# Performance work log

Hardware: AMD Instinct MI355X
Metric: run time of the kernel (lower is better)

The kernel has to match this reference:

```python
import jax, jax.numpy as jnp
import numpy as np

TEMPERATURE = 0.1
NORMALIZE = True


def setup_inputs() -> dict:
    key = jax.random.key(0)
    k1, k2 = jax.random.split(key)
    B, D = 4096, 512
    return {
        "z_i": jax.random.normal(k1, (B, D), dtype=jnp.float32),
        "z_j": jax.random.normal(k2, (B, D), dtype=jnp.float32),
    }


def _l2norm(x):
    return x / jnp.sqrt(jnp.sum(x * x, axis=-1, keepdims=True))


def reference(z_i, z_j):
    if NORMALIZE:
        z_i = _l2norm(z_i)
        z_j = _l2norm(z_j)
    B = z_i.shape[0]

    inv_t = 1.0 / TEMPERATURE
    logits_aa = (z_i @ z_i.T) * inv_t  # [B, B]
    logits_bb = (z_j @ z_j.T) * inv_t
    logits_ab = (z_i @ z_j.T) * inv_t
    logits_ba = (z_j @ z_i.T) * inv_t

    # Static off-diagonal column indices: row i keeps cols 0..B-1 except i,
    # in ascending order (matches torch boolean-mask row-major extraction).
    j = jnp.arange(B - 1)[None, :]
    i = jnp.arange(B)[:, None]
    idx = j + (j >= i)  # [B, B-1] int32

    take = lambda m: jnp.take_along_axis(m, idx, axis=1)  # [B, B-1]

    pos = jnp.concatenate([jnp.diagonal(logits_ab), jnp.diagonal(logits_ba)])[:, None]  # [2B, 1]
    neg_a = jnp.concatenate([take(logits_aa), take(logits_ab)], axis=1)  # [B, 2(B-1)]
    neg_b = jnp.concatenate([take(logits_ba), take(logits_bb)], axis=1)
    neg = jnp.concatenate([neg_a, neg_b], axis=0)  # [2B, 2(B-1)]

    logits = jnp.concatenate([pos, neg], axis=1)  # [2B, 2B-1]
    logp = jax.nn.log_softmax(logits, axis=1)
    # Original forward uses labels = torch.ones(2B).long() -> target class 1.
    loss = -jnp.mean(logp[:, 1])
    return loss
```

## Files before the change

### kernel.cpp

```cpp
#include <hip/hip_runtime.h>
#include <hip/hip_bf16.h>
#include <hip/hip_fp8.h>


#define BB 4096
#define DD 512
#define NN 8192
#define TILE 128
#define KB 128
#define NBLK 2080

typedef __attribute__((ext_vector_type(4))) float f32x4;

#define AS1 __attribute__((address_space(1)))
#define AS3 __attribute__((address_space(3)))
static __device__ __forceinline__ void gload_lds16(const void* g, void* l) {
    __builtin_amdgcn_global_load_lds((const AS1 void*)g, (AS3 void*)l, 16, 0, 0);
}

__global__ __launch_bounds__(256)
void normalize_kernel(const float* __restrict__ zi, const float* __restrict__ zj,
                      unsigned char* __restrict__ M, float* __restrict__ rowsum) {
    const int wave = threadIdx.x >> 6;
    const int lane = threadIdx.x & 63;
    const int row  = blockIdx.x * 4 + wave;
    if (threadIdx.x < 4) rowsum[blockIdx.x * 4 + threadIdx.x] = 0.f;
    const float* src = (row < BB) ? (zi + (size_t)row * DD)
                                  : (zj + (size_t)(row - BB) * DD);
    float4 v0 = ((const float4*)src)[lane * 2 + 0];
    float4 v1 = ((const float4*)src)[lane * 2 + 1];
    float ss = v0.x*v0.x + v0.y*v0.y + v0.z*v0.z + v0.w*v0.w
             + v1.x*v1.x + v1.y*v1.y + v1.z*v1.z + v1.w*v1.w;
    #pragma unroll
    for (int off = 1; off <= 32; off <<= 1) ss += __shfl_xor(ss, off);
    const float inv = rsqrtf(ss);
    const float vals[8] = {v0.x*inv, v0.y*inv, v0.z*inv, v0.w*inv,
                           v1.x*inv, v1.y*inv, v1.z*inv, v1.w*inv};
    union { long u; unsigned char b[8]; } pk;
    #pragma unroll
    for (int j = 0; j < 8; ++j)
        pk.b[j] = __hip_cvt_float_to_fp8(vals[j], __HIP_SATFINITE, __HIP_E4M3);
    ((long*)(M + (size_t)row * DD))[lane] = pk.u;
}

__global__ __launch_bounds__(256, 4)
void gram_lse_kernel(const unsigned char* __restrict__ Mg,
                     float* __restrict__ rowsum, float* __restrict__ targets) {
    __shared__ __align__(16) char As[TILE * KB];
    __shared__ __align__(16) char Bs[TILE * KB];

    const int d = blockIdx.x;
    const int p = (d & 7) * 260 + (d >> 3);
    int by = (int)((sqrtf(8.0f * (float)p + 1.0f) - 1.0f) * 0.5f);
    while ((by + 1) * (by + 2) / 2 <= p) ++by;
    while (by * (by + 1) / 2 > p) --by;
    const int bx = p - by * (by + 1) / 2;

    const int rowBase = bx * TILE;
    const int colBase = by * TILE;
    const bool diag = (bx == by);
    const int tid  = threadIdx.x;
    const int wave = tid >> 6;
    const int lane = tid & 63;
    const int wr = (wave >> 1) * 64;
    const int wc = (wave & 1) * 64;
    const int l15 = lane & 15;
    const int l4  = lane >> 4;

    const int sg  = (tid & 7) ^ ((tid >> 3) & 7);
    const int sr0 = tid >> 3;
    const unsigned char* gA0 = Mg + (size_t)(rowBase + sr0) * DD + sg * 16;
    const unsigned char* gB0 = Mg + (size_t)(colBase + sr0) * DD + sg * 16;
    char* lA0 = As + tid * 16;
    char* lB0 = Bs + tid * 16;

    const int r7 = l15 & 7;
    const int qh = l4 >> 1, ql = l4 & 1;
    const int aoff0 = (wr + l15) * KB + ql * 8;
    const int boff0 = (wc + l15) * KB + ql * 8;
    const char* BsP = diag ? As : Bs;

    f32x4 acc[4][4] = {};

    for (int k0 = 0; k0 < DD; k0 += KB) {
        __syncthreads();
        #pragma unroll
        for (int i = 0; i < 4; ++i)
            gload_lds16(gA0 + k0 + (size_t)i * 32 * DD, lA0 + i * 4096);
        if (!diag) {
            #pragma unroll
            for (int i = 0; i < 4; ++i)
                gload_lds16(gB0 + k0 + (size_t)i * 32 * DD, lB0 + i * 4096);
        }
        __syncthreads();
        #pragma unroll
        for (int ks = 0; ks < 4; ++ks) {
            const int so = ((((ks << 1) | qh) ^ r7) << 4);
            long a[4], b[4];
            #pragma unroll
            for (int mi = 0; mi < 4; ++mi)
                a[mi] = *(const long*)(As + aoff0 + mi * 2048 + so);
            #pragma unroll
            for (int ni = 0; ni < 4; ++ni)
                b[ni] = *(const long*)(BsP + boff0 + ni * 2048 + so);
            #pragma unroll
            for (int mi = 0; mi < 4; ++mi)
                #pragma unroll
                for (int ni = 0; ni < 4; ++ni)
                    acc[mi][ni] = __builtin_amdgcn_mfma_f32_16x16x32_fp8_fp8(
                        a[mi], b[ni], acc[mi][ni], 0, 0, 0);
        }
    }

    float cs[4] = {0.f, 0.f, 0.f, 0.f};
    #pragma unroll
    for (int mi = 0; mi < 4; ++mi) {
        float rs[4] = {0.f, 0.f, 0.f, 0.f};
        #pragma unroll
        for (int ni = 0; ni < 4; ++ni) {
            const int gcol = colBase + wc + ni * 16 + l15;
            #pragma unroll
            for (int r = 0; r < 4; ++r) {
                const int grow = rowBase + wr + mi * 16 + l4 * 4 + r;
                float logit = 10.f * acc[mi][ni][r];
                float e = __expf(logit - 10.f);
                if (grow == gcol) e = 0.f;
                rs[r] += e;
                cs[ni] += e;
                if (rowBase == 0 && grow < 2) {
                    const int j0 = ((gcol & (BB - 1)) == 0) ? 1 : 0;
                    if (grow == j0) targets[gcol] = logit;
                }
            }
        }
        #pragma unroll
        for (int m = 1; m <= 8; m <<= 1)
            #pragma unroll
            for (int r = 0; r < 4; ++r)
                rs[r] += __shfl_xor(rs[r], m);
        if (l15 == 0) {
            #pragma unroll
            for (int r = 0; r < 4; ++r)
                atomicAdd(&rowsum[rowBase + wr + mi * 16 + l4 * 4 + r], rs[r]);
        }
    }
    if (!diag) {
        #pragma unroll
        for (int ni = 0; ni < 4; ++ni) {
            cs[ni] += __shfl_xor(cs[ni], 16);
            cs[ni] += __shfl_xor(cs[ni], 32);
        }
        if (l4 == 0) {
            #pragma unroll
            for (int ni = 0; ni < 4; ++ni)
                atomicAdd(&rowsum[colBase + wc + ni * 16 + l15], cs[ni]);
        }
    }
}

__global__ __launch_bounds__(1024)
void finalize_kernel(const float* __restrict__ rowsum,
                     const float* __restrict__ targets, float* __restrict__ out) {
    const int tid = threadIdx.x;
    float s = 0.f;
    #pragma unroll
    for (int t = tid; t < NN; t += 1024)
        s += targets[t] - 10.f - __logf(rowsum[t]);
    #pragma unroll
    for (int off = 1; off <= 32; off <<= 1) s += __shfl_xor(s, off);
    __shared__ float red[16];
    if ((tid & 63) == 0) red[tid >> 6] = s;
    __syncthreads();
    if (tid == 0) {
        float t = 0.f;
        #pragma unroll
        for (int i = 0; i < 16; ++i) t += red[i];
        out[0] = -t / (float)NN;
    }
}

extern "C" void kernel_launch(void* const* d_in, const int* in_sizes, int n_in,
                              void* d_out, int out_size, void* d_ws, size_t ws_size,
                              hipStream_t stream) {
    const float* zi = (const float*)d_in[0];
    const float* zj = (const float*)d_in[1];

    unsigned char* M = (unsigned char*)d_ws;
    float* rowsum  = (float*)((char*)d_ws + (size_t)NN * DD);
    float* targets = rowsum + NN;
    float* out = (float*)d_out;

    normalize_kernel<<<NN / 4, 256, 0, stream>>>(zi, zj, M, rowsum);
    gram_lse_kernel<<<NBLK, 256, 0, stream>>>(M, rowsum, targets);
    finalize_kernel<<<1, 1024, 0, stream>>>(rowsum, targets, out);
}
```

Before: 101.0 us.

## Double-buffer LDS tiles in gram kernel and use exp2 in epilogue

Splits the shared-memory A/B tiles into two buffers and prefetches the next K slice with direct global-to-LDS loads while MFMAs consume the current one, removing one barrier per iteration. The epilogue exponential is folded into a single fma plus hardware exp2. Doubling LDS lowers the occupancy bound from 4 to 2 blocks per CU. Correctness relies on the barrier waiting for the async LDS loads to complete.

```diff
diff --git a/kernel.cpp b/kernel.cpp
--- a/kernel.cpp
+++ b/kernel.cpp
@@ -43,11 +43,11 @@
     ((long*)(M + (size_t)row * DD))[lane] = pk.u;
 }
 
-__global__ __launch_bounds__(256, 4)
+__global__ __launch_bounds__(256, 2)
 void gram_lse_kernel(const unsigned char* __restrict__ Mg,
                      float* __restrict__ rowsum, float* __restrict__ targets) {
-    __shared__ __align__(16) char As[TILE * KB];
-    __shared__ __align__(16) char Bs[TILE * KB];
+    __shared__ __align__(16) char As[2][TILE * KB];
+    __shared__ __align__(16) char Bs[2][TILE * KB];
 
     const int d = blockIdx.x;
     const int p = (d & 7) * 260 + (d >> 3);
@@ -71,38 +71,55 @@
     const int sr0 = tid >> 3;
     const unsigned char* gA0 = Mg + (size_t)(rowBase + sr0) * DD + sg * 16;
     const unsigned char* gB0 = Mg + (size_t)(colBase + sr0) * DD + sg * 16;
-    char* lA0 = As + tid * 16;
-    char* lB0 = Bs + tid * 16;
 
     const int r7 = l15 & 7;
     const int qh = l4 >> 1, ql = l4 & 1;
     const int aoff0 = (wr + l15) * KB + ql * 8;
     const int boff0 = (wc + l15) * KB + ql * 8;
-    const char* BsP = diag ? As : Bs;
 
     f32x4 acc[4][4] = {};
 
-    for (int k0 = 0; k0 < DD; k0 += KB) {
+    {
+        char* lA = As[0] + tid * 16;
+        #pragma unroll
+        for (int i = 0; i < 4; ++i)
+            gload_lds16(gA0 + (size_t)i * 32 * DD, lA + i * 4096);
+        if (!diag) {
+            char* lB = Bs[0] + tid * 16;
+            #pragma unroll
+            for (int i = 0; i < 4; ++i)
+                gload_lds16(gB0 + (size_t)i * 32 * DD, lB + i * 4096);
+        }
+    }
+
+    #pragma unroll
+    for (int t = 0; t < DD / KB; ++t) {
         __syncthreads();
-        #pragma unroll
-        for (int i = 0; i < 4; ++i)
-            gload_lds16(gA0 + k0 + (size_t)i * 32 * DD, lA0 + i * 4096);
-        if (!diag) {
+        if (t < DD / KB - 1) {
+            const int k0 = (t + 1) * KB;
+            char* lA = As[(t + 1) & 1] + tid * 16;
             #pragma unroll
             for (int i = 0; i < 4; ++i)
-                gload_lds16(gB0 + k0 + (size_t)i * 32 * DD, lB0 + i * 4096);
-        }
-        __syncthreads();
+                gload_lds16(gA0 + k0 + (size_t)i * 32 * DD, lA + i * 4096);
+            if (!diag) {
+                char* lB = Bs[(t + 1) & 1] + tid * 16;
+                #pragma unroll
+                for (int i = 0; i < 4; ++i)
+                    gload_lds16(gB0 + k0 + (size_t)i * 32 * DD, lB + i * 4096);
+            }
+        }
+        const char* Asrc = As[t & 1];
+        const char* Bsrc = diag ? Asrc : Bs[t & 1];
         #pragma unroll
         for (int ks = 0; ks < 4; ++ks) {
             const int so = ((((ks << 1) | qh) ^ r7) << 4);
             long a[4], b[4];
             #pragma unroll
             for (int mi = 0; mi < 4; ++mi)
-                a[mi] = *(const long*)(As + aoff0 + mi * 2048 + so);
+                a[mi] = *(const long*)(Asrc + aoff0 + mi * 2048 + so);
             #pragma unroll
             for (int ni = 0; ni < 4; ++ni)
-                b[ni] = *(const long*)(BsP + boff0 + ni * 2048 + so);
+                b[ni] = *(const long*)(Bsrc + boff0 + ni * 2048 + so);
             #pragma unroll
             for (int mi = 0; mi < 4; ++mi)
                 #pragma unroll
@@ -112,6 +129,7 @@
         }
     }
 
+    const float C10 = 14.42695040888963f;
     float cs[4] = {0.f, 0.f, 0.f, 0.f};
     #pragma unroll
     for (int mi = 0; mi < 4; ++mi) {
@@ -122,14 +140,13 @@
             #pragma unroll
             for (int r = 0; r < 4; ++r) {
                 const int grow = rowBase + wr + mi * 16 + l4 * 4 + r;
-                float logit = 10.f * acc[mi][ni][r];
-                float e = __expf(logit - 10.f);
+                float e = __builtin_amdgcn_exp2f(fmaf(acc[mi][ni][r], C10, -C10));
                 if (grow == gcol) e = 0.f;
                 rs[r] += e;
                 cs[ni] += e;
                 if (rowBase == 0 && grow < 2) {
                     const int j0 = ((gcol & (BB - 1)) == 0) ? 1 : 0;
-                    if (grow == j0) targets[gcol] = logit;
+                    if (grow == j0) targets[gcol] = 10.f * acc[mi][ni][r];
                 }
             }
         }
```

New measurement: 110.0 us. 8.9% more time.

## Switch Gram kernel to 32x32x64 scaled FP8 MFMA with A in registers

Applied to the files above, without the earlier changes.

Replaces the 16x16x32 FP8 MFMA tiled loop over K with the MI355 32x32x64 f8f6f4 scaled MFMA. The whole 128xD B tile is staged once into LDS with an XOR swizzle, and each wave keeps its 32 A rows in registers loaded straight from global memory, which removes the K-loop barriers and the A LDS traffic. The epilogue uses exp2 with a folded constant. The cost is more registers (occupancy bound dropped to 2) and a larger 64KB LDS footprint.

```diff
diff --git a/kernel.cpp b/kernel.cpp
--- a/kernel.cpp
+++ b/kernel.cpp
@@ -7,10 +7,12 @@
 #define DD 512
 #define NN 8192
 #define TILE 128
-#define KB 128
 #define NBLK 2080
 
-typedef __attribute__((ext_vector_type(4))) float f32x4;
+typedef __attribute__((ext_vector_type(4)))  float f32x4;
+typedef __attribute__((ext_vector_type(16))) float f32x16;
+typedef __attribute__((ext_vector_type(4)))  int   i32x4;
+typedef __attribute__((ext_vector_type(8)))  int   i32x8;
 
 #define AS1 __attribute__((address_space(1)))
 #define AS3 __attribute__((address_space(3)))
@@ -43,11 +45,10 @@
     ((long*)(M + (size_t)row * DD))[lane] = pk.u;
 }
 
-__global__ __launch_bounds__(256, 4)
+__global__ __launch_bounds__(256, 2)
 void gram_lse_kernel(const unsigned char* __restrict__ Mg,
                      float* __restrict__ rowsum, float* __restrict__ targets) {
-    __shared__ __align__(16) char As[TILE * KB];
-    __shared__ __align__(16) char Bs[TILE * KB];
+    __shared__ __align__(16) char Bs[TILE * DD];
 
     const int d = blockIdx.x;
     const int p = (d & 7) * 260 + (d >> 3);
@@ -62,98 +63,84 @@
     const int tid  = threadIdx.x;
     const int wave = tid >> 6;
     const int lane = tid & 63;
-    const int wr = (wave >> 1) * 64;
-    const int wc = (wave & 1) * 64;
-    const int l15 = lane & 15;
-    const int l4  = lane >> 4;
+    const int l31 = lane & 31;
+    const int h0  = lane >> 5;
 
-    const int sg  = (tid & 7) ^ ((tid >> 3) & 7);
-    const int sr0 = tid >> 3;
-    const unsigned char* gA0 = Mg + (size_t)(rowBase + sr0) * DD + sg * 16;
-    const unsigned char* gB0 = Mg + (size_t)(colBase + sr0) * DD + sg * 16;
-    char* lA0 = As + tid * 16;
-    char* lB0 = Bs + tid * 16;
+    #pragma unroll
+    for (int i = 0; i < 16; ++i) {
+        const int row = i * 8 + (tid >> 5);
+        const int sg  = (tid & 31) ^ (row & 31);
+        gload_lds16(Mg + (size_t)(colBase + row) * DD + sg * 16,
+                    Bs + ((size_t)i * 256 + tid) * 16);
+    }
 
-    const int r7 = l15 & 7;
-    const int qh = l4 >> 1, ql = l4 & 1;
-    const int aoff0 = (wr + l15) * KB + ql * 8;
-    const int boff0 = (wc + l15) * KB + ql * 8;
-    const char* BsP = diag ? As : Bs;
+    const unsigned char* Arow = Mg + (size_t)(rowBase + wave * 32 + l31) * DD + h0 * 32;
+    i32x4 a4[16];
+    #pragma unroll
+    for (int t2 = 0; t2 < 16; ++t2)
+        a4[t2] = *(const i32x4*)(Arow + (t2 >> 1) * 64 + (t2 & 1) * 16);
 
-    f32x4 acc[4][4] = {};
+    __syncthreads();
 
-    for (int k0 = 0; k0 < DD; k0 += KB) {
-        __syncthreads();
+    f32x16 acc[4] = {};
+    const int rb0 = l31 * DD;
+    #pragma unroll
+    for (int t = 0; t < 8; ++t) {
+        const int g0 = t * 4 + h0 * 2;
+        const int p0 = (g0 ^ l31) * 16;
+        const int p1 = ((g0 ^ 1) ^ l31) * 16;
+        const i32x8 a = __builtin_shufflevector(a4[2 * t], a4[2 * t + 1],
+                                                0, 1, 2, 3, 4, 5, 6, 7);
         #pragma unroll
-        for (int i = 0; i < 4; ++i)
-            gload_lds16(gA0 + k0 + (size_t)i * 32 * DD, lA0 + i * 4096);
-        if (!diag) {
-            #pragma unroll
-            for (int i = 0; i < 4; ++i)
-                gload_lds16(gB0 + k0 + (size_t)i * 32 * DD, lB0 + i * 4096);
-        }
-        __syncthreads();
-        #pragma unroll
-        for (int ks = 0; ks < 4; ++ks) {
-            const int so = ((((ks << 1) | qh) ^ r7) << 4);
-            long a[4], b[4];
-            #pragma unroll
-            for (int mi = 0; mi < 4; ++mi)
-                a[mi] = *(const long*)(As + aoff0 + mi * 2048 + so);
-            #pragma unroll
-            for (int ni = 0; ni < 4; ++ni)
-                b[ni] = *(const long*)(BsP + boff0 + ni * 2048 + so);
-            #pragma unroll
-            for (int mi = 0; mi < 4; ++mi)
-                #pragma unroll
-                for (int ni = 0; ni < 4; ++ni)
-                    acc[mi][ni] = __builtin_amdgcn_mfma_f32_16x16x32_fp8_fp8(
-                        a[mi], b[ni], acc[mi][ni], 0, 0, 0);
+        for (int ni = 0; ni < 4; ++ni) {
+            const char* rbase = Bs + rb0 + ni * 32 * DD;
+            i32x4 lo = *(const i32x4*)(rbase + p0);
+            i32x4 hi = *(const i32x4*)(rbase + p1);
+            i32x8 b = __builtin_shufflevector(lo, hi, 0, 1, 2, 3, 4, 5, 6, 7);
+            acc[ni] = __builtin_amdgcn_mfma_scale_f32_32x32x64_f8f6f4(
+                a, b, acc[ni], 0, 0, 0, 0x7F7F7F7F, 0, 0x7F7F7F7F);
         }
     }
 
-    float cs[4] = {0.f, 0.f, 0.f, 0.f};
+    const float C10 = 14.42695040888963f;
+    float rs[16] = {};
+    float cs[4]  = {};
     #pragma unroll
-    for (int mi = 0; mi < 4; ++mi) {
-        float rs[4] = {0.f, 0.f, 0.f, 0.f};
+    for (int ni = 0; ni < 4; ++ni) {
+        const int gcol = colBase + ni * 32 + l31;
         #pragma unroll
-        for (int ni = 0; ni < 4; ++ni) {
-            const int gcol = colBase + wc + ni * 16 + l15;
-            #pragma unroll
-            for (int r = 0; r < 4; ++r) {
-                const int grow = rowBase + wr + mi * 16 + l4 * 4 + r;
-                float logit = 10.f * acc[mi][ni][r];
-                float e = __expf(logit - 10.f);
-                if (grow == gcol) e = 0.f;
-                rs[r] += e;
-                cs[ni] += e;
-                if (rowBase == 0 && grow < 2) {
-                    const int j0 = ((gcol & (BB - 1)) == 0) ? 1 : 0;
-                    if (grow == j0) targets[gcol] = logit;
-                }
+        for (int r = 0; r < 16; ++r) {
+            const int lrow = (r & 3) + 8 * (r >> 2) + 4 * h0;
+            const int grow = rowBase + wave * 32 + lrow;
+            float e = __builtin_amdgcn_exp2f(fmaf(acc[ni][r], C10, -C10));
+            if (grow == gcol) e = 0.f;
+            rs[r] += e;
+            cs[ni] += e;
+            if (rowBase == 0 && grow < 2) {
+                const int j0 = ((gcol & (BB - 1)) == 0) ? 1 : 0;
+                if (grow == j0) targets[gcol] = 10.f * acc[ni][r];
             }
         }
+    }
+    #pragma unroll
+    for (int m = 1; m <= 16; m <<= 1)
         #pragma unroll
-        for (int m = 1; m <= 8; m <<= 1)
-            #pragma unroll
-            for (int r = 0; r < 4; ++r)
-                rs[r] += __shfl_xor(rs[r], m);
-        if (l15 == 0) {
-            #pragma unroll
-            for (int r = 0; r < 4; ++r)
-                atomicAdd(&rowsum[rowBase + wr + mi * 16 + l4 * 4 + r], rs[r]);
-        }
+        for (int r = 0; r < 16; ++r)
+            rs[r] += __shfl_xor(rs[r], m);
+    if (l31 == 0) {
+        #pragma unroll
+        for (int r = 0; r < 16; ++r)
+            atomicAdd(&rowsum[rowBase + wave * 32
+                              + (r & 3) + 8 * (r >> 2) + 4 * h0], rs[r]);
     }
     if (!diag) {
         #pragma unroll
-        for (int ni = 0; ni < 4; ++ni) {
-            cs[ni] += __shfl_xor(cs[ni], 16);
+        for (int ni = 0; ni < 4; ++ni)
             cs[ni] += __shfl_xor(cs[ni], 32);
-        }
-        if (l4 == 0) {
+        if (h0 == 0) {
             #pragma unroll
             for (int ni = 0; ni < 4; ++ni)
-                atomicAdd(&rowsum[colBase + wc + ni * 16 + l15], cs[ni]);
+                atomicAdd(&rowsum[colBase + ni * 32 + l31], cs[ni]);
         }
     }
 }
```

Measured after the change: 108.8 us. 7.8% more time.
